# Kernel tuning notes

Hardware: AMD Instinct MI355X
Metric: run time of the kernel (lower is better)

The kernel has to match this reference:

```python
import jax, jax.numpy as jnp
import numpy as np

N_NODES = 50000
N_EDGES = 800000
NFEAT, NHID, NCLASS = 512, 256, 64


def _glorot(key, fan_in, fan_out):
    # mimics kipf-style uniform init: U(-1/sqrt(fan_out), 1/sqrt(fan_out))
    stdv = 1.0 / np.sqrt(fan_out)
    return jax.random.uniform(key, (fan_in, fan_out), jnp.float32, -stdv, stdv)


def setup_inputs() -> dict:
    key = jax.random.key(0)
    ks = jax.random.split(key, 8)
    x = jax.random.normal(ks[0], (N_NODES, NFEAT), jnp.float32)
    edge_src = jax.random.randint(ks[1], (N_EDGES,), 0, N_NODES, jnp.int32)
    edge_dst = jax.random.randint(ks[2], (N_EDGES,), 0, N_NODES, jnp.int32)
    edge_weight = jax.random.uniform(ks[3], (N_EDGES,), jnp.float32)
    W1 = _glorot(ks[4], NFEAT, NHID)
    b1 = jax.random.uniform(ks[5], (NHID,), jnp.float32, -1.0 / np.sqrt(NHID), 1.0 / np.sqrt(NHID))
    W2 = _glorot(ks[6], NHID, NCLASS)
    b2 = jax.random.uniform(ks[7], (NCLASS,), jnp.float32, -1.0 / np.sqrt(NCLASS), 1.0 / np.sqrt(NCLASS))
    return {"x": x, "W1": W1, "b1": b1, "W2": W2, "b2": b2,
            "edge_weight": edge_weight, "edge_src": edge_src, "edge_dst": edge_dst}


def _spmm(edge_src, edge_dst, edge_weight, support):
    # adj @ support with adj given as COO edge list: out[d] += w * support[s]
    msgs = support[edge_src] * edge_weight[:, None]  # [E, F]
    return jax.ops.segment_sum(msgs, edge_dst, num_segments=N_NODES)


def reference(x, W1, b1, W2, b2, edge_weight, edge_src, edge_dst):
    # layer 1: GraphConvolution -> ReLU (dropout identity in eval mode)
    h = _spmm(edge_src, edge_dst, edge_weight, x @ W1) + b1
    h = jax.nn.relu(h)
    # layer 2: GraphConvolution -> log_softmax over classes
    logits = _spmm(edge_src, edge_dst, edge_weight, h @ W2) + b2
    return jax.nn.log_softmax(logits, axis=1)
```

## Files before the change

### kernel.cpp

```cpp
#include <hip/hip_runtime.h>
#include <cstdint>


typedef unsigned short u16;
typedef unsigned int u32;
typedef __attribute__((ext_vector_type(8))) short bf16x8;
typedef __attribute__((ext_vector_type(4))) float f32x4;

#define N_NODES 50000
#define N_EDGES 800000
#define NFEAT 512
#define NHID 256
#define NCLASS 64
#define CSTRIDE 64
#define DEGS 16

#define SB  391
#define GB1 782
#define PW1B 512
#define PW2B 64
#define DEGZB 196

__device__ __forceinline__ float bf2f(u16 h) {
    union { u32 u; float f; } c; c.u = ((u32)h) << 16; return c.f;
}
__device__ __forceinline__ u16 f2bf(float f) {
    union { float f; u32 u; } c; c.f = f;
    u32 u = c.u;
    return (u16)((u + 0x7fffu + ((u >> 16) & 1u)) >> 16);
}
__device__ __forceinline__ u32 pk2(float a, float b) {
    return (u32)f2bf(a) | ((u32)f2bf(b) << 16);
}

__device__ __forceinline__ void async16(const void* g, void* l) {
    __builtin_amdgcn_global_load_lds(
        (const __attribute__((address_space(1))) void*)(uintptr_t)g,
        (__attribute__((address_space(3))) void*)(uintptr_t)l, 16, 0, 0);
}


__global__ __launch_bounds__(256) void prep0_kernel(
    const float* __restrict__ W1, u16* __restrict__ W1T,
    const float* __restrict__ W2, u16* __restrict__ W2T,
    int* __restrict__ deg) {
    int b = blockIdx.x;
    if (b < PW1B) {
        int idx = b * 256 + threadIdx.x;
        int n = idx >> 9, k = idx & 511;
        W1T[idx] = f2bf(W1[(size_t)k * NHID + n]);
    } else if (b < PW1B + PW2B) {
        int idx = (b - PW1B) * 256 + threadIdx.x;
        int n = idx >> 8, k = idx & 255;
        W2T[idx] = f2bf(W2[(size_t)k * NCLASS + n]);
    } else {
        int base = (b - PW1B - PW2B) * 4096 + threadIdx.x * 16;
        if (base < N_NODES * DEGS) {
            int4 z = make_int4(0, 0, 0, 0);
            int4* p = (int4*)(deg + base);
            p[0] = z; p[1] = z; p[2] = z; p[3] = z;
        }
    }
}


template <int MT, int NT, int WCOLS, int K, bool ACVT>
__device__ __forceinline__ void gemm_body(const void* __restrict__ Av,
                                          const u16* __restrict__ BT,
                                          u16* __restrict__ C, int M,
                                          int bid, u16* lds) {
    constexpr int WROWS = 4 / WCOLS;
    constexpr int RT = MT / (16 * WROWS);
    constexpr int CT = NT / (16 * WCOLS);
    u16* As = lds;
    u16* Bs = lds + MT * 64;

    const int tid  = threadIdx.x;
    const int wv   = tid >> 6, lane = tid & 63;
    const int lm   = lane & 15, quad = lane >> 4;
    const int wrow = wv / WCOLS, wcol = wv % WCOLS;
    const int m0   = bid * MT;
    const int co0 = ((0 * 4 + quad) ^ (lm & 7)) * 8;
    const int co1 = ((1 * 4 + quad) ^ (lm & 7)) * 8;

    f32x4 acc[RT][CT];
    #pragma unroll
    for (int r = 0; r < RT; ++r)
        #pragma unroll
        for (int c = 0; c < CT; ++c) acc[r][c] = (f32x4){0.f, 0.f, 0.f, 0.f};

    for (int k0 = 0; k0 < K; k0 += 64) {
        if constexpr (ACVT) {
            static_assert(MT == 64, "ACVT staging assumes MT==64 (16 elems/thread)");
            const float* Af = (const float*)Av;
            int row = tid >> 2, ko = (tid & 3) * 16;
            int gr = m0 + row; if (gr > M - 1) gr = M - 1;
            const float4* gp = (const float4*)(Af + (size_t)gr * K + k0 + ko);
            float4 f0 = gp[0], f1 = gp[1], f2 = gp[2], f3 = gp[3];
            #pragma unroll
            for (int i = 0; i < NT / 32; ++i) {
                int c = i * 256 + tid;
                int n = c >> 3, kb = c & 7;
                async16(BT + (size_t)n * K + k0 + ((kb ^ (n & 7)) * 8), Bs + c * 8);
            }
            u32 p[8] = {pk2(f0.x, f0.y), pk2(f0.z, f0.w), pk2(f1.x, f1.y), pk2(f1.z, f1.w),
                        pk2(f2.x, f2.y), pk2(f2.z, f2.w), pk2(f3.x, f3.y), pk2(f3.z, f3.w)};
            int ch0 = (2 * (tid & 3))     ^ (row & 7);
            int ch1 = (2 * (tid & 3) + 1) ^ (row & 7);
            *(int4*)(As + row * 64 + ch0 * 8) = *(int4*)&p[0];
            *(int4*)(As + row * 64 + ch1 * 8) = *(int4*)&p[4];
        } else {
            const u16* A = (const u16*)Av;
            #pragma unroll
            for (int i = 0; i < NT / 32; ++i) {
                int c = i * 256 + tid;
                int n = c >> 3, kb = c & 7;
                async16(BT + (size_t)n * K + k0 + ((kb ^ (n & 7)) * 8), Bs + c * 8);
            }
            #pragma unroll
            for (int i = 0; i < MT / 32; ++i) {
                int c = i * 256 + tid;
                int row = c >> 3, kb = c & 7;
                int gr = m0 + row; if (gr > M - 1) gr = M - 1;
                async16(A + (size_t)gr * K + k0 + ((kb ^ (row & 7)) * 8), As + c * 8);
            }
        }
        __syncthreads();

        #pragma unroll
        for (int kk = 0; kk < 2; ++kk) {
            const int co = kk ? co1 : co0;
            bf16x8 af[RT], bfv[CT];
            #pragma unroll
            for (int rt = 0; rt < RT; ++rt) {
                int row = wrow * (RT * 16) + rt * 16 + lm;
                af[rt] = *(const bf16x8*)(As + row * 64 + co);
            }
            #pragma unroll
            for (int ct = 0; ct < CT; ++ct) {
                int n = wcol * CT * 16 + ct * 16 + lm;
                bfv[ct] = *(const bf16x8*)(Bs + n * 64 + co);
            }
            #pragma unroll
            for (int rt = 0; rt < RT; ++rt)
                #pragma unroll
                for (int ct = 0; ct < CT; ++ct)
                    acc[rt][ct] = __builtin_amdgcn_mfma_f32_16x16x32_bf16(
                        af[rt], bfv[ct], acc[rt][ct], 0, 0, 0);
        }
        __syncthreads();
    }

    #pragma unroll
    for (int rt = 0; rt < RT; ++rt)
        #pragma unroll
        for (int ct = 0; ct < CT; ++ct) {
            int col = wcol * CT * 16 + ct * 16 + lm;
            #pragma unroll
            for (int r = 0; r < 4; ++r) {
                int row = wrow * (RT * 16) + rt * 16 + quad * 4 + r;
                lds[row * NT + col] = f2bf(acc[rt][ct][r]);
            }
        }
    __syncthreads();
    constexpr int NC = MT * NT / 2048;
    #pragma unroll
    for (int i = 0; i < NC; ++i) {
        int c = i * 256 + tid;
        int row = (c * 8) / NT;
        if (m0 + row < M)
            *(int4*)(C + (size_t)m0 * NT + c * 8) = *(const int4*)(lds + c * 8);
    }
}


__global__ __launch_bounds__(256) void gemm1_scatter_kernel(
    const float* __restrict__ x, const u16* __restrict__ W1T, u16* __restrict__ S1,
    const int* __restrict__ esrc, const int* __restrict__ edst,
    const float* __restrict__ ew, int* __restrict__ deg, u32* __restrict__ csr) {
    __shared__ __align__(16) u16 lds[(64 + 256) * 64];
    int b = blockIdx.x;
    if (b < SB) {
        int e0 = (b * 256 + threadIdx.x) * 8;
        if (e0 < N_EDGES) {
            int4 d0 = *(const int4*)(edst + e0),  d1 = *(const int4*)(edst + e0 + 4);
            int4 s0 = *(const int4*)(esrc + e0),  s1 = *(const int4*)(esrc + e0 + 4);
            float4 w0 = *(const float4*)(ew + e0), w1 = *(const float4*)(ew + e0 + 4);
            int d[8] = {d0.x, d0.y, d0.z, d0.w, d1.x, d1.y, d1.z, d1.w};
            int s[8] = {s0.x, s0.y, s0.z, s0.w, s1.x, s1.y, s1.z, s1.w};
            float w[8] = {w0.x, w0.y, w0.z, w0.w, w1.x, w1.y, w1.z, w1.w};
            int r[8];
            #pragma unroll
            for (int i = 0; i < 8; ++i)
                r[i] = atomicAdd(&deg[d[i] * DEGS], 1);
            #pragma unroll
            for (int i = 0; i < 8; ++i)
                if (r[i] < CSTRIDE)
                    csr[(size_t)d[i] * CSTRIDE + r[i]] = (u32)s[i] | ((u32)f2bf(w[i]) << 16);
        }
    } else {
        gemm_body<64, 256, 4, NFEAT, true>(x, W1T, S1, N_NODES, b - SB, lds);
    }
}


__global__ __launch_bounds__(256) void gemm2_kernel(const u16* __restrict__ H,
                                                    const u16* __restrict__ W2T,
                                                    u16* __restrict__ S2, int M) {
    __shared__ __align__(16) u16 lds[(128 + 64) * 64];
    gemm_body<128, 64, 2, NHID, false>(H, W2T, S2, M, blockIdx.x, lds);
}


__global__ __launch_bounds__(256) void spmm_bias_relu_kernel(
    const u16* __restrict__ S, const int* __restrict__ deg,
    const u32* __restrict__ csr, const float* __restrict__ bias,
    u16* __restrict__ H, int n) {
    int node = blockIdx.x * 4 + (threadIdx.x >> 6);
    if (node >= n) return;
    node = __builtin_amdgcn_readfirstlane(node);
    int lane = threadIdx.x & 63;
    int beg = node * CSTRIDE;
    int end = beg + deg[node * DEGS];
    float a0 = 0.f, a1 = 0.f, a2 = 0.f, a3 = 0.f;
    int j = beg;
    for (; j + 8 <= end; j += 8) {
        u32 e[8];
        #pragma unroll
        for (int i = 0; i < 8; ++i) e[i] = csr[j + i];
        ushort4 v[8];
        #pragma unroll
        for (int i = 0; i < 8; ++i)
            v[i] = *(const ushort4*)(S + (size_t)(e[i] & 0xFFFFu) * NHID + lane * 4);
        #pragma unroll
        for (int i = 0; i < 8; ++i) {
            float w = bf2f((u16)(e[i] >> 16));
            a0 += w * bf2f(v[i].x); a1 += w * bf2f(v[i].y);
            a2 += w * bf2f(v[i].z); a3 += w * bf2f(v[i].w);
        }
    }
    for (; j < end; ++j) {
        u32 e0 = csr[j];
        float w = bf2f((u16)(e0 >> 16));
        ushort4 v0 = *(const ushort4*)(S + (size_t)(e0 & 0xFFFFu) * NHID + lane * 4);
        a0 += w * bf2f(v0.x); a1 += w * bf2f(v0.y);
        a2 += w * bf2f(v0.z); a3 += w * bf2f(v0.w);
    }
    float4 bv = *(const float4*)(bias + lane * 4);
    a0 = fmaxf(a0 + bv.x, 0.f);
    a1 = fmaxf(a1 + bv.y, 0.f);
    a2 = fmaxf(a2 + bv.z, 0.f);
    a3 = fmaxf(a3 + bv.w, 0.f);
    ushort4 o;
    o.x = f2bf(a0); o.y = f2bf(a1); o.z = f2bf(a2); o.w = f2bf(a3);
    *(ushort4*)(H + (size_t)node * NHID + lane * 4) = o;
}


__global__ __launch_bounds__(256) void spmm_bias_lsm_kernel(
    const u16* __restrict__ S, const int* __restrict__ deg,
    const u32* __restrict__ csr, const float* __restrict__ bias,
    float* __restrict__ out, int n) {
    int node = blockIdx.x * 4 + (threadIdx.x >> 6);
    if (node >= n) return;
    node = __builtin_amdgcn_readfirstlane(node);
    int lane = threadIdx.x & 63;
    int beg = node * CSTRIDE;
    int end = beg + deg[node * DEGS];
    float acc = 0.f;
    int j = beg;
    for (; j + 8 <= end; j += 8) {
        u32 e[8];
        #pragma unroll
        for (int i = 0; i < 8; ++i) e[i] = csr[j + i];
        u16 v[8];
        #pragma unroll
        for (int i = 0; i < 8; ++i)
            v[i] = S[(size_t)(e[i] & 0xFFFFu) * NCLASS + lane];
        #pragma unroll
        for (int i = 0; i < 8; ++i)
            acc += bf2f((u16)(e[i] >> 16)) * bf2f(v[i]);
    }
    for (; j < end; ++j) {
        u32 e0 = csr[j];
        acc += bf2f((u16)(e0 >> 16)) * bf2f(S[(size_t)(e0 & 0xFFFFu) * NCLASS + lane]);
    }

    float x = acc + bias[lane];
    float m = x;
    #pragma unroll
    for (int off = 32; off > 0; off >>= 1) m = fmaxf(m, __shfl_xor(m, off));
    float e = expf(x - m);
    float ssum = e;
    #pragma unroll
    for (int off = 32; off > 0; off >>= 1) ssum += __shfl_xor(ssum, off);
    out[(size_t)node * NCLASS + lane] = x - m - logf(ssum);
}


extern "C" void kernel_launch(void* const* d_in, const int* in_sizes, int n_in,
                              void* d_out, int out_size, void* d_ws, size_t ws_size,
                              hipStream_t stream) {
    const float* x  = (const float*)d_in[0];
    const float* W1 = (const float*)d_in[1];
    const float* b1 = (const float*)d_in[2];
    const float* W2 = (const float*)d_in[3];
    const float* b2 = (const float*)d_in[4];
    const float* ew = (const float*)d_in[5];
    const int* esrc = (const int*)d_in[6];
    const int* edst = (const int*)d_in[7];
    float* out = (float*)d_out;

    char* ws = (char*)d_ws;
    size_t off = 0;
    auto take = [&](size_t bytes) -> void* {
        off = (off + 255) & ~(size_t)255;
        void* p = ws + off;
        off += bytes;
        return p;
    };
    u16* S1  = (u16*)take((size_t)N_NODES * NHID * 2);
    u16* H   = (u16*)take((size_t)N_NODES * NHID * 2);
    u16* S2  = (u16*)take((size_t)N_NODES * NCLASS * 2);
    u16* W1T = (u16*)take((size_t)NHID * NFEAT * 2);
    u16* W2T = (u16*)take((size_t)NCLASS * NHID * 2);
    int* deg = (int*)take((size_t)N_NODES * DEGS * 4);
    u32* csr = (u32*)take((size_t)N_NODES * CSTRIDE * 4);
    (void)ws_size; (void)in_sizes; (void)n_in; (void)out_size;

    prep0_kernel<<<PW1B + PW2B + DEGZB, 256, 0, stream>>>(W1, W1T, W2, W2T, deg);
    gemm1_scatter_kernel<<<SB + GB1, 256, 0, stream>>>(x, W1T, S1, esrc, edst, ew,
                                                       deg, csr);
    spmm_bias_relu_kernel<<<(N_NODES + 3) / 4, 256, 0, stream>>>(
        S1, deg, csr, b1, H, N_NODES);
    gemm2_kernel<<<(N_NODES + 127) / 128, 256, 0, stream>>>(H, W2T, S2, N_NODES);
    spmm_bias_lsm_kernel<<<(N_NODES + 3) / 4, 256, 0, stream>>>(
        S2, deg, csr, b2, out, N_NODES);
}
```

Before: 298.8 us.

## Fuse layer-1 SpMM+bias+ReLU with layer-2 GEMM via LDS-resident hidden tile

Merges the first-layer sparse aggregation (with bias and ReLU) and the H@W2 GEMM into one kernel. Each block aggregates 16 nodes into a swizzled LDS tile, then runs MFMA against W2T chunks streamed into LDS, writing S2 directly. This drops the global H buffer write/read and one launch, at the cost of smaller blocks (16 rows), reloading W2T per block, and extra syncs.

```diff
diff --git a/kernel.cpp b/kernel.cpp
--- a/kernel.cpp
+++ b/kernel.cpp
@@ -20,6 +20,7 @@
 #define PW1B 512
 #define PW2B 64
 #define DEGZB 196
+#define FNB 3125
 
 __device__ __forceinline__ float bf2f(u16 h) {
     union { u32 u; float f; } c; c.u = ((u32)h) << 16; return c.f;
@@ -204,56 +205,89 @@
 }
 
 
-__global__ __launch_bounds__(256) void gemm2_kernel(const u16* __restrict__ H,
-                                                    const u16* __restrict__ W2T,
-                                                    u16* __restrict__ S2, int M) {
-    __shared__ __align__(16) u16 lds[(128 + 64) * 64];
-    gemm_body<128, 64, 2, NHID, false>(H, W2T, S2, M, blockIdx.x, lds);
-}
-
-
-__global__ __launch_bounds__(256) void spmm_bias_relu_kernel(
+__global__ __launch_bounds__(256) void spmm1_gemm2_kernel(
     const u16* __restrict__ S, const int* __restrict__ deg,
-    const u32* __restrict__ csr, const float* __restrict__ bias,
-    u16* __restrict__ H, int n) {
-    int node = blockIdx.x * 4 + (threadIdx.x >> 6);
-    if (node >= n) return;
-    node = __builtin_amdgcn_readfirstlane(node);
-    int lane = threadIdx.x & 63;
-    int beg = node * CSTRIDE;
-    int end = beg + deg[node * DEGS];
-    float a0 = 0.f, a1 = 0.f, a2 = 0.f, a3 = 0.f;
-    int j = beg;
-    for (; j + 8 <= end; j += 8) {
-        u32 e[8];
-        #pragma unroll
-        for (int i = 0; i < 8; ++i) e[i] = csr[j + i];
-        ushort4 v[8];
-        #pragma unroll
-        for (int i = 0; i < 8; ++i)
-            v[i] = *(const ushort4*)(S + (size_t)(e[i] & 0xFFFFu) * NHID + lane * 4);
-        #pragma unroll
-        for (int i = 0; i < 8; ++i) {
-            float w = bf2f((u16)(e[i] >> 16));
-            a0 += w * bf2f(v[i].x); a1 += w * bf2f(v[i].y);
-            a2 += w * bf2f(v[i].z); a3 += w * bf2f(v[i].w);
-        }
-    }
-    for (; j < end; ++j) {
-        u32 e0 = csr[j];
-        float w = bf2f((u16)(e0 >> 16));
-        ushort4 v0 = *(const ushort4*)(S + (size_t)(e0 & 0xFFFFu) * NHID + lane * 4);
-        a0 += w * bf2f(v0.x); a1 += w * bf2f(v0.y);
-        a2 += w * bf2f(v0.z); a3 += w * bf2f(v0.w);
-    }
-    float4 bv = *(const float4*)(bias + lane * 4);
-    a0 = fmaxf(a0 + bv.x, 0.f);
-    a1 = fmaxf(a1 + bv.y, 0.f);
-    a2 = fmaxf(a2 + bv.z, 0.f);
-    a3 = fmaxf(a3 + bv.w, 0.f);
-    ushort4 o;
-    o.x = f2bf(a0); o.y = f2bf(a1); o.z = f2bf(a2); o.w = f2bf(a3);
-    *(ushort4*)(H + (size_t)node * NHID + lane * 4) = o;
+    const u32* __restrict__ csr, const float* __restrict__ bias1,
+    const u16* __restrict__ W2T, u16* __restrict__ S2) {
+    __shared__ __align__(16) u16 Hs[16 * 256];
+    __shared__ __align__(16) u16 Bs[64 * 64];
+
+    const int tid  = threadIdx.x;
+    const int wv   = tid >> 6, lane = tid & 63;
+    const int lm   = lane & 15, quad = lane >> 4;
+    const int b    = blockIdx.x;
+
+    float4 bv = *(const float4*)(bias1 + lane * 4);
+
+    #pragma unroll
+    for (int it = 0; it < 4; ++it) {
+        int lrow = wv * 4 + it;
+        int node = __builtin_amdgcn_readfirstlane(b * 16 + lrow);
+        int beg = node * CSTRIDE;
+        int end = beg + deg[node * DEGS];
+        float a0 = 0.f, a1 = 0.f, a2 = 0.f, a3 = 0.f;
+        int j = beg;
+        for (; j + 8 <= end; j += 8) {
+            u32 e[8];
+            #pragma unroll
+            for (int i = 0; i < 8; ++i) e[i] = csr[j + i];
+            ushort4 v[8];
+            #pragma unroll
+            for (int i = 0; i < 8; ++i)
+                v[i] = *(const ushort4*)(S + (size_t)(e[i] & 0xFFFFu) * NHID + lane * 4);
+            #pragma unroll
+            for (int i = 0; i < 8; ++i) {
+                float w = bf2f((u16)(e[i] >> 16));
+                a0 += w * bf2f(v[i].x); a1 += w * bf2f(v[i].y);
+                a2 += w * bf2f(v[i].z); a3 += w * bf2f(v[i].w);
+            }
+        }
+        for (; j < end; ++j) {
+            u32 e0 = csr[j];
+            float w = bf2f((u16)(e0 >> 16));
+            ushort4 v0 = *(const ushort4*)(S + (size_t)(e0 & 0xFFFFu) * NHID + lane * 4);
+            a0 += w * bf2f(v0.x); a1 += w * bf2f(v0.y);
+            a2 += w * bf2f(v0.z); a3 += w * bf2f(v0.w);
+        }
+        a0 = fmaxf(a0 + bv.x, 0.f);
+        a1 = fmaxf(a1 + bv.y, 0.f);
+        a2 = fmaxf(a2 + bv.z, 0.f);
+        a3 = fmaxf(a3 + bv.w, 0.f);
+        int ch = (lane >> 1) ^ (lrow & 7);
+        u32* dp = (u32*)(Hs + lrow * 256 + ch * 8 + (lane & 1) * 4);
+        dp[0] = pk2(a0, a1);
+        dp[1] = pk2(a2, a3);
+    }
+    __syncthreads();
+
+    f32x4 acc = (f32x4){0.f, 0.f, 0.f, 0.f};
+    for (int k0 = 0; k0 < NHID; k0 += 64) {
+        #pragma unroll
+        for (int i = 0; i < 2; ++i) {
+            int c = i * 256 + tid;
+            int n = c >> 3, kb = c & 7;
+            async16(W2T + (size_t)n * NHID + k0 + ((kb ^ (n & 7)) * 8), Bs + c * 8);
+        }
+        __syncthreads();
+        #pragma unroll
+        for (int kk = 0; kk < 2; ++kk) {
+            int ca = ((k0 >> 3) + kk * 4 + quad) ^ (lm & 7);
+            bf16x8 af = *(const bf16x8*)(Hs + lm * 256 + ca * 8);
+            int n = wv * 16 + lm;
+            int cb = (kk * 4 + quad) ^ (n & 7);
+            bf16x8 bf = *(const bf16x8*)(Bs + n * 64 + cb * 8);
+            acc = __builtin_amdgcn_mfma_f32_16x16x32_bf16(af, bf, acc, 0, 0, 0);
+        }
+        __syncthreads();
+    }
+
+    #pragma unroll
+    for (int r = 0; r < 4; ++r) {
+        int row = quad * 4 + r;
+        Hs[row * 64 + wv * 16 + lm] = f2bf(acc[r]);
+    }
+    __syncthreads();
+    *(ushort4*)(S2 + (size_t)b * 1024 + tid * 4) = *(const ushort4*)(Hs + tid * 4);
 }
 
 
@@ -320,7 +354,6 @@
         return p;
     };
     u16* S1  = (u16*)take((size_t)N_NODES * NHID * 2);
-    u16* H   = (u16*)take((size_t)N_NODES * NHID * 2);
     u16* S2  = (u16*)take((size_t)N_NODES * NCLASS * 2);
     u16* W1T = (u16*)take((size_t)NHID * NFEAT * 2);
     u16* W2T = (u16*)take((size_t)NCLASS * NHID * 2);
@@ -331,9 +364,7 @@
     prep0_kernel<<<PW1B + PW2B + DEGZB, 256, 0, stream>>>(W1, W1T, W2, W2T, deg);
     gemm1_scatter_kernel<<<SB + GB1, 256, 0, stream>>>(x, W1T, S1, esrc, edst, ew,
                                                        deg, csr);
-    spmm_bias_relu_kernel<<<(N_NODES + 3) / 4, 256, 0, stream>>>(
-        S1, deg, csr, b1, H, N_NODES);
-    gemm2_kernel<<<(N_NODES + 127) / 128, 256, 0, stream>>>(H, W2T, S2, N_NODES);
+    spmm1_gemm2_kernel<<<FNB, 256, 0, stream>>>(S1, deg, csr, b1, W2T, S2);
     spmm_bias_lsm_kernel<<<(N_NODES + 3) / 4, 256, 0, stream>>>(
         S2, deg, csr, b2, out, N_NODES);
 }
```

Result: no change. 298.8 us (-0.0%).
